# Optimization experiments

Hardware: AMD Instinct MI355X
Metric: run time of the kernel (lower is better)

## Reference

```python
import jax, jax.numpy as jnp
import numpy as np

B, N, E, H, L = 1, 1024, 32, 1024, 8  # batch, num concepts, dim_edge, dim_hidden, stack_len


def setup_inputs() -> dict:
    key = jax.random.key(0)
    k = jax.random.split(key, 12)
    vision_feat = jax.random.normal(k[0], (B, 36, H), jnp.float32)   # unused by forward
    feat = jax.random.normal(k[1], (B, N - 1, N, E), jnp.float32)
    feat_edge = jax.random.normal(k[2], (B, 1, N, E), jnp.float32)
    c_i = jax.random.normal(k[3], (B, H), jnp.float32)
    relation_mask = jnp.ones((B, N), jnp.float32)                    # only its size is read
    att_stack = jax.random.uniform(k[4], (B, N, N, L), dtype=jnp.float32)
    sp = jax.random.uniform(k[5], (B, L), dtype=jnp.float32)
    stack_ptr = sp / jnp.sum(sp, axis=-1, keepdims=True)             # soft stack pointer
    mem_in = jax.random.normal(k[6], (B, H), jnp.float32)
    mono_mask = (jax.random.uniform(k[7], (B, N, N, 1)) > 0.5).astype(jnp.float32)
    cross_mask = jax.random.uniform(k[8], (E,), dtype=jnp.float32)
    w_c = jax.random.normal(k[9], (E, H), jnp.float32) / np.sqrt(H).astype(np.float32)
    b_c = jax.random.normal(k[10], (E,), jnp.float32) * 0.01
    return {"vision_feat": vision_feat, "feat": feat, "feat_edge": feat_edge,
            "c_i": c_i, "relation_mask": relation_mask, "att_stack": att_stack,
            "stack_ptr": stack_ptr, "mem_in": mem_in, "mono_mask": mono_mask,
            "cross_mask": cross_mask, "w_c": w_c, "b_c": b_c}


def reference(vision_feat, feat, feat_edge, c_i, relation_mask, att_stack,
              stack_ptr, mem_in, mono_mask, cross_mask, w_c, b_c):
    b = feat_edge.shape[0]
    # query = map_c(c_i).view(B,1,1,-1).expand_as(feat_edge)
    query = (c_i @ w_c.T + b_c).reshape(b, 1, 1, -1)
    query = jnp.broadcast_to(query, feat_edge.shape)                 # (B,1,N,E)
    I = jnp.concatenate([query, feat], axis=1)                       # (B,N,N,E)
    # Fusion: -(x-y)^2 + relu(x+y), feat_edge broadcasts over dim1
    elt_prod = -(I - feat_edge) ** 2 + jax.nn.relu(I + feat_edge)    # (B,N,N,E)
    weit_matrix = mono_mask * elt_prod                               # (B,N,N,E)
    # soft stack read + permute(0,2,1): att_in[b,y,x] = sum_l att_stack[b,x,y,l]*ptr[b,l]
    att_in = jnp.einsum('bxyl,bl->byx', att_stack, stack_ptr)        # (B,N,N)
    # (att_in @ weit_matrix) @ cross_mask, then permute(0,2,1).
    # Contract the edge dim first (mathematically identical by linearity).
    wv = jnp.einsum('bmye,e->bmy', weit_matrix, cross_mask)          # (B,N,N)
    att_out = jnp.einsum('bxy,bmy->bxm', att_in, wv)                 # (B,N,N)
    # max-normalize with detached norm clamped to >= 1
    norm = jax.lax.stop_gradient(jnp.max(att_out, axis=1, keepdims=True))
    norm = jnp.where(norm <= 1, jnp.ones_like(norm), norm)
    att_out = att_out / norm
    # soft stack write
    ptr = stack_ptr[:, None, None, :]                                # (B,1,1,L)
    att_stack_new = att_out[..., None] * ptr + att_stack * (1 - ptr) # (B,N,N,L)
    return att_stack_new, stack_ptr, jnp.zeros_like(mem_in)
```

## Files before the change

kernel.cpp:

```cpp
#include <hip/hip_runtime.h>
#include <math.h>

#define N 1024
#define E 32
#define L 8
#define NN ((size_t)N * N)

using short8 = __attribute__((ext_vector_type(8))) short;
using f32x4v = __attribute__((ext_vector_type(4))) float;

__device__ inline ushort2 split_bf16(float v) {
  unsigned ui = __float_as_uint(v);
  ushort h = (ushort)(ui >> 16);
  float hv = __uint_as_float((unsigned)h << 16);
  float r = v - hv;
  ushort l = (ushort)(__float_as_uint(r) >> 16);
  return make_ushort2(h, l);
}

__device__ inline void gload16(const void* g, void* l) {
  __builtin_amdgcn_global_load_lds(
      (const __attribute__((address_space(1))) unsigned int*)g,
      (__attribute__((address_space(3))) unsigned int*)l, 16, 0, 0);
}

__global__ __launch_bounds__(256) void k_prep(
    const float* __restrict__ feat, const float* __restrict__ fe,
    const float* __restrict__ mono, const float* __restrict__ cm,
    const float* __restrict__ c_i, const float* __restrict__ w_c,
    const float* __restrict__ b_c,
    const float* __restrict__ att_stack, const float* __restrict__ ptr,
    ushort* __restrict__ wv_h, ushort* __restrict__ wv_l,
    ushort* __restrict__ Pt_h, ushort* __restrict__ Pt_l,
    float* __restrict__ out_tail) {
  __shared__ __align__(16) float qsm[32];
  __shared__ ushort Ts[2][64][66];
  int tid = threadIdx.x;
  int b = blockIdx.x;
  if (b < 8192) {
    int seg = tid & 7;
    int rl = tid >> 3;
    bool qblock = (b < 8);
    if (qblock) {
      int e = tid >> 3, r = tid & 7;
      float s = 0.f;
      for (int h = r; h < N; h += 8) s += c_i[h] * w_c[e * N + h];
      s += __shfl_down(s, 4, 8);
      s += __shfl_down(s, 2, 8);
      s += __shfl_down(s, 1, 8);
      if (r == 0) qsm[e] = s + b_c[e];
      __syncthreads();
    }
    float4 c = *(const float4*)(cm + seg * 4);
    float4 qa;
    if (qblock) qa = *((const float4*)qsm + seg);
    #pragma unroll
    for (int it = 0; it < 4; ++it) {
      int gid = b * 128 + it * 32 + rl;
      int m = gid >> 10;
      int y = gid & (N - 1);
      float4 a;
      if (qblock) {
        a = qa;
      } else {
        a = *(const float4*)(feat + ((size_t)(m - 1) * N + y) * E + seg * 4);
      }
      float4 f = *(const float4*)(fe + (size_t)y * E + seg * 4);
      float dx = a.x - f.x, dy = a.y - f.y, dz = a.z - f.z, dw = a.w - f.w;
      float s = c.x * (fmaxf(a.x + f.x, 0.f) - dx * dx)
              + c.y * (fmaxf(a.y + f.y, 0.f) - dy * dy)
              + c.z * (fmaxf(a.z + f.z, 0.f) - dz * dz)
              + c.w * (fmaxf(a.w + f.w, 0.f) - dw * dw);
      s += __shfl_down(s, 4, 8);
      s += __shfl_down(s, 2, 8);
      s += __shfl_down(s, 1, 8);
      if (seg == 0) {
        float v = mono[gid] * s;
        ushort2 hl = split_bf16(v);
        wv_h[gid] = hl.x;
        wv_l[gid] = hl.y;
      }
    }
  } else if (b < 8448) {
    int b2 = b - 8192;
    int j0 = (b2 >> 4) * 64;
    int i0 = (b2 & 15) * 64;
    float p0 = ptr[0], p1 = ptr[1], p2 = ptr[2], p3 = ptr[3];
    float p4 = ptr[4], p5 = ptr[5], p6 = ptr[6], p7 = ptr[7];
    int w = tid >> 6, lane = tid & 63;
    #pragma unroll 4
    for (int r = 0; r < 16; ++r) {
      int jl = r * 4 + w;
      int il = lane;
      const float4* a =
          (const float4*)(att_stack + ((size_t)(j0 + jl) * N + i0 + il) * L);
      float4 a0 = a[0], a1 = a[1];
      float s = a0.x * p0 + a0.y * p1 + a0.z * p2 + a0.w * p3
              + a1.x * p4 + a1.y * p5 + a1.z * p6 + a1.w * p7;
      ushort2 hl = split_bf16(s);
      Ts[0][il][jl] = hl.x;
      Ts[1][il][jl] = hl.y;
    }
    __syncthreads();
    int il = tid >> 2, cc = tid & 3;
    size_t o = (size_t)(i0 + il) * N + j0 + cc * 16;
    {
      const uint* sp = (const uint*)&Ts[0][il][cc * 16];
      uint4 d0 = {sp[0], sp[1], sp[2], sp[3]};
      uint4 d1 = {sp[4], sp[5], sp[6], sp[7]};
      *(uint4*)&Pt_h[o] = d0;
      *(uint4*)&Pt_h[o + 8] = d1;
    }
    {
      const uint* sp = (const uint*)&Ts[1][il][cc * 16];
      uint4 d0 = {sp[0], sp[1], sp[2], sp[3]};
      uint4 d1 = {sp[4], sp[5], sp[6], sp[7]};
      *(uint4*)&Pt_l[o] = d0;
      *(uint4*)&Pt_l[o + 8] = d1;
    }
  } else {
    if (tid < 8) out_tail[tid] = ptr[tid];
    for (int i = tid; i < N; i += 256) out_tail[8 + i] = 0.f;
  }
}

__global__ __launch_bounds__(256) void k_mm(
    const ushort* __restrict__ Pt_h, const ushort* __restrict__ Pt_l,
    const ushort* __restrict__ wv_h, const ushort* __restrict__ wv_l,
    float* __restrict__ C, float* __restrict__ normp) {
  __shared__ ushort As[2][2][64][32];
  __shared__ ushort Bs[2][2][64][32];
  __shared__ float nm[64][17];
  int tid = threadIdx.x;
  int lane = tid & 63, w = tid >> 6;
  int x0 = blockIdx.x * 64, m0 = blockIdx.y * 64;
  int srow = w * 16 + (lane >> 2);
  int gsrc = (((lane & 3) ^ ((lane >> 3) & 3))) * 8;
  const ushort* gAh = Pt_h + (size_t)(x0 + srow) * N + gsrc;
  const ushort* gAl = Pt_l + (size_t)(x0 + srow) * N + gsrc;
  const ushort* gBh = wv_h + (size_t)(m0 + srow) * N + gsrc;
  const ushort* gBl = wv_l + (size_t)(m0 + srow) * N + gsrc;
  int fr = w * 16 + (lane & 15);
  int fn = lane & 15;
  int grn = ((lane >> 4) ^ ((lane >> 1) & 3)) << 4;
  f32x4v acc[4];
  #pragma unroll
  for (int t = 0; t < 4; ++t) acc[t] = (f32x4v){0.f, 0.f, 0.f, 0.f};
  gload16(gAh, &As[0][0][w * 16][0]);
  gload16(gAl, &As[0][1][w * 16][0]);
  gload16(gBh, &Bs[0][0][w * 16][0]);
  gload16(gBl, &Bs[0][1][w * 16][0]);
  #pragma unroll 2
  for (int kt = 0; kt < 32; ++kt) {
    int cur = kt & 1;
    __syncthreads();
    if (kt < 31) {
      int nxt = cur ^ 1;
      gload16(gAh + (kt + 1) * 32, &As[nxt][0][w * 16][0]);
      gload16(gAl + (kt + 1) * 32, &As[nxt][1][w * 16][0]);
      gload16(gBh + (kt + 1) * 32, &Bs[nxt][0][w * 16][0]);
      gload16(gBl + (kt + 1) * 32, &Bs[nxt][1][w * 16][0]);
    }
    const char* aB0 = (const char*)&As[cur][0][0][0];
    const char* aB1 = (const char*)&As[cur][1][0][0];
    short8 Ah = *(const short8*)(aB0 + fr * 64 + grn);
    short8 Al = *(const short8*)(aB1 + fr * 64 + grn);
    const char* bB0 = (const char*)&Bs[cur][0][0][0];
    const char* bB1 = (const char*)&Bs[cur][1][0][0];
    #pragma unroll
    for (int t = 0; t < 4; ++t) {
      short8 Bh = *(const short8*)(bB0 + (t * 16 + fn) * 64 + grn);
      short8 Bl = *(const short8*)(bB1 + (t * 16 + fn) * 64 + grn);
      acc[t] = __builtin_amdgcn_mfma_f32_16x16x32_bf16(Ah, Bh, acc[t], 0, 0, 0);
      acc[t] = __builtin_amdgcn_mfma_f32_16x16x32_bf16(Ah, Bl, acc[t], 0, 0, 0);
      acc[t] = __builtin_amdgcn_mfma_f32_16x16x32_bf16(Al, Bh, acc[t], 0, 0, 0);
    }
  }
  int orow = x0 + w * 16 + (lane >> 4) * 4;
  int ocol = m0 + fn;
  int cidx = w * 4 + (lane >> 4);
  #pragma unroll
  for (int t = 0; t < 4; ++t) {
    float mx = -INFINITY;
    #pragma unroll
    for (int r = 0; r < 4; ++r) {
      float v = acc[t][r];
      C[(size_t)(orow + r) * N + ocol + t * 16] = v;
      mx = fmaxf(mx, v);
    }
    nm[t * 16 + fn][cidx] = mx;
  }
  __syncthreads();
  if (tid < 64) {
    float mx = nm[tid][0];
    #pragma unroll
    for (int j = 1; j < 16; ++j) mx = fmaxf(mx, nm[tid][j]);
    normp[(size_t)blockIdx.x * N + m0 + tid] = mx;
  }
}

__global__ __launch_bounds__(256) void k_fin(
    const float* __restrict__ C, const float* __restrict__ normp,
    const float* __restrict__ att_stack, const float* __restrict__ ptr,
    float* __restrict__ out) {
  int gid = blockIdx.x * 256 + threadIdx.x;
  int m = gid & (N - 1);
  float mx = normp[m];
  #pragma unroll
  for (int xg = 1; xg < 16; ++xg)
    mx = fmaxf(mx, normp[(size_t)xg * N + m]);
  float nrm = (mx <= 1.f) ? 1.f : mx;
  float a = C[gid] / nrm;
  const float4* s = (const float4*)(att_stack + (size_t)gid * L);
  float4 s0 = s[0], s1 = s[1];
  float p0 = ptr[0], p1 = ptr[1], p2 = ptr[2], p3 = ptr[3];
  float p4 = ptr[4], p5 = ptr[5], p6 = ptr[6], p7 = ptr[7];
  float4 o0, o1;
  o0.x = a * p0 + s0.x * (1.f - p0);
  o0.y = a * p1 + s0.y * (1.f - p1);
  o0.z = a * p2 + s0.z * (1.f - p2);
  o0.w = a * p3 + s0.w * (1.f - p3);
  o1.x = a * p4 + s1.x * (1.f - p4);
  o1.y = a * p5 + s1.y * (1.f - p5);
  o1.z = a * p6 + s1.z * (1.f - p6);
  o1.w = a * p7 + s1.w * (1.f - p7);
  float4* o = (float4*)(out + (size_t)gid * L);
  o[0] = o0;
  o[1] = o1;
}

extern "C" void kernel_launch(void* const* d_in, const int* in_sizes, int n_in,
                              void* d_out, int out_size, void* d_ws, size_t ws_size,
                              hipStream_t stream) {
  const float* feat      = (const float*)d_in[1];
  const float* feat_edge = (const float*)d_in[2];
  const float* c_i       = (const float*)d_in[3];
  const float* att_stack = (const float*)d_in[5];
  const float* stack_ptr = (const float*)d_in[6];
  const float* mono_mask = (const float*)d_in[8];
  const float* cross_mask= (const float*)d_in[9];
  const float* w_c       = (const float*)d_in[10];
  const float* b_c       = (const float*)d_in[11];

  float* out = (float*)d_out;

  ushort* wv_h = (ushort*)d_ws;
  ushort* wv_l = wv_h + NN;
  ushort* Pt_h = wv_l + NN;
  ushort* Pt_l = Pt_h + NN;
  float*  C    = (float*)(Pt_l + NN);
  float*  normp= C + NN;

  float* out_tail = out + NN * L;

  k_prep<<<8449, 256, 0, stream>>>(feat, feat_edge, mono_mask, cross_mask,
                                   c_i, w_c, b_c, att_stack, stack_ptr,
                                   wv_h, wv_l, Pt_h, Pt_l, out_tail);
  dim3 mmgrid(16, 16);
  k_mm<<<mmgrid, 256, 0, stream>>>(Pt_h, Pt_l, wv_h, wv_l, C, normp);
  k_fin<<<4096, 256, 0, stream>>>(C, normp, att_stack, stack_ptr, out);
}
```

Measured before the change: 280.3 us.

## Load GEMM fragments directly into registers with 4-stage prefetch; split finalize per half-row

The split-bf16 GEMM no longer stages A/B tiles through LDS with global_load_lds and a barrier on every k-step. Each wave now loads its MFMA fragments straight from global memory into registers, keeping four k-steps in flight as a software pipeline, which removes the LDS traffic and __syncthreads. In exchange, register pressure rises sharply (4 stages of 10 short8 vectors), and the B fragments are reloaded redundantly by each of the four waves instead of being shared through LDS. The finalize kernel now uses two threads per element, each doing one float4, doubling the thread count to get more coalesced and parallel memory access.

```diff
diff --git a/kernel.cpp b/kernel.cpp
--- a/kernel.cpp
+++ b/kernel.cpp
@@ -16,12 +16,6 @@
   float r = v - hv;
   ushort l = (ushort)(__float_as_uint(r) >> 16);
   return make_ushort2(h, l);
-}
-
-__device__ inline void gload16(const void* g, void* l) {
-  __builtin_amdgcn_global_load_lds(
-      (const __attribute__((address_space(1))) unsigned int*)g,
-      (__attribute__((address_space(3))) unsigned int*)l, 16, 0, 0);
 }
 
 __global__ __launch_bounds__(256) void k_prep(
@@ -128,56 +122,60 @@
     const ushort* __restrict__ Pt_h, const ushort* __restrict__ Pt_l,
     const ushort* __restrict__ wv_h, const ushort* __restrict__ wv_l,
     float* __restrict__ C, float* __restrict__ normp) {
-  __shared__ ushort As[2][2][64][32];
-  __shared__ ushort Bs[2][2][64][32];
   __shared__ float nm[64][17];
   int tid = threadIdx.x;
   int lane = tid & 63, w = tid >> 6;
   int x0 = blockIdx.x * 64, m0 = blockIdx.y * 64;
-  int srow = w * 16 + (lane >> 2);
-  int gsrc = (((lane & 3) ^ ((lane >> 3) & 3))) * 8;
-  const ushort* gAh = Pt_h + (size_t)(x0 + srow) * N + gsrc;
-  const ushort* gAl = Pt_l + (size_t)(x0 + srow) * N + gsrc;
-  const ushort* gBh = wv_h + (size_t)(m0 + srow) * N + gsrc;
-  const ushort* gBl = wv_l + (size_t)(m0 + srow) * N + gsrc;
-  int fr = w * 16 + (lane & 15);
-  int fn = lane & 15;
-  int grn = ((lane >> 4) ^ ((lane >> 1) & 3)) << 4;
+  int fr = lane & 15;
+  int fk = (lane >> 4) * 8;
+  const ushort* pAh = Pt_h + (size_t)(x0 + w * 16 + fr) * N + fk;
+  const ushort* pAl = Pt_l + (size_t)(x0 + w * 16 + fr) * N + fk;
+  size_t br0 = (size_t)(m0 + 0 * 16 + fr) * N + fk;
+  size_t br1 = (size_t)(m0 + 1 * 16 + fr) * N + fk;
+  size_t br2 = (size_t)(m0 + 2 * 16 + fr) * N + fk;
+  size_t br3 = (size_t)(m0 + 3 * 16 + fr) * N + fk;
+
+  short8 Ah[4], Al[4], Bh[4][4], Bl[4][4];
+
+#define LOADK(s, kt)                                                   \
+  do {                                                                 \
+    const int ko = (kt) * 32;                                          \
+    Ah[s] = *(const short8*)(pAh + ko);                                \
+    Al[s] = *(const short8*)(pAl + ko);                                \
+    Bh[s][0] = *(const short8*)(wv_h + br0 + ko);                      \
+    Bl[s][0] = *(const short8*)(wv_l + br0 + ko);                      \
+    Bh[s][1] = *(const short8*)(wv_h + br1 + ko);                      \
+    Bl[s][1] = *(const short8*)(wv_l + br1 + ko);                      \
+    Bh[s][2] = *(const short8*)(wv_h + br2 + ko);                      \
+    Bl[s][2] = *(const short8*)(wv_l + br2 + ko);                      \
+    Bh[s][3] = *(const short8*)(wv_h + br3 + ko);                      \
+    Bl[s][3] = *(const short8*)(wv_l + br3 + ko);                      \
+  } while (0)
+
   f32x4v acc[4];
   #pragma unroll
   for (int t = 0; t < 4; ++t) acc[t] = (f32x4v){0.f, 0.f, 0.f, 0.f};
-  gload16(gAh, &As[0][0][w * 16][0]);
-  gload16(gAl, &As[0][1][w * 16][0]);
-  gload16(gBh, &Bs[0][0][w * 16][0]);
-  gload16(gBl, &Bs[0][1][w * 16][0]);
-  #pragma unroll 2
+
+  LOADK(0, 0);
+  LOADK(1, 1);
+  LOADK(2, 2);
+  LOADK(3, 3);
+
+  #pragma unroll
   for (int kt = 0; kt < 32; ++kt) {
-    int cur = kt & 1;
-    __syncthreads();
-    if (kt < 31) {
-      int nxt = cur ^ 1;
-      gload16(gAh + (kt + 1) * 32, &As[nxt][0][w * 16][0]);
-      gload16(gAl + (kt + 1) * 32, &As[nxt][1][w * 16][0]);
-      gload16(gBh + (kt + 1) * 32, &Bs[nxt][0][w * 16][0]);
-      gload16(gBl + (kt + 1) * 32, &Bs[nxt][1][w * 16][0]);
-    }
-    const char* aB0 = (const char*)&As[cur][0][0][0];
-    const char* aB1 = (const char*)&As[cur][1][0][0];
-    short8 Ah = *(const short8*)(aB0 + fr * 64 + grn);
-    short8 Al = *(const short8*)(aB1 + fr * 64 + grn);
-    const char* bB0 = (const char*)&Bs[cur][0][0][0];
-    const char* bB1 = (const char*)&Bs[cur][1][0][0];
+    const int s = kt & 3;
     #pragma unroll
     for (int t = 0; t < 4; ++t) {
-      short8 Bh = *(const short8*)(bB0 + (t * 16 + fn) * 64 + grn);
-      short8 Bl = *(const short8*)(bB1 + (t * 16 + fn) * 64 + grn);
-      acc[t] = __builtin_amdgcn_mfma_f32_16x16x32_bf16(Ah, Bh, acc[t], 0, 0, 0);
-      acc[t] = __builtin_amdgcn_mfma_f32_16x16x32_bf16(Ah, Bl, acc[t], 0, 0, 0);
-      acc[t] = __builtin_amdgcn_mfma_f32_16x16x32_bf16(Al, Bh, acc[t], 0, 0, 0);
-    }
-  }
+      acc[t] = __builtin_amdgcn_mfma_f32_16x16x32_bf16(Ah[s], Bh[s][t], acc[t], 0, 0, 0);
+      acc[t] = __builtin_amdgcn_mfma_f32_16x16x32_bf16(Ah[s], Bl[s][t], acc[t], 0, 0, 0);
+      acc[t] = __builtin_amdgcn_mfma_f32_16x16x32_bf16(Al[s], Bh[s][t], acc[t], 0, 0, 0);
+    }
+    if (kt < 28) LOADK(s, kt + 4);
+  }
+#undef LOADK
+
   int orow = x0 + w * 16 + (lane >> 4) * 4;
-  int ocol = m0 + fn;
+  int ocol = m0 + fr;
   int cidx = w * 4 + (lane >> 4);
   #pragma unroll
   for (int t = 0; t < 4; ++t) {
@@ -188,7 +186,7 @@
       C[(size_t)(orow + r) * N + ocol + t * 16] = v;
       mx = fmaxf(mx, v);
     }
-    nm[t * 16 + fn][cidx] = mx;
+    nm[t * 16 + fr][cidx] = mx;
   }
   __syncthreads();
   if (tid < 64) {
@@ -203,30 +201,24 @@
     const float* __restrict__ C, const float* __restrict__ normp,
     const float* __restrict__ att_stack, const float* __restrict__ ptr,
     float* __restrict__ out) {
-  int gid = blockIdx.x * 256 + threadIdx.x;
+  int f = blockIdx.x * 256 + threadIdx.x;
+  int gid = f >> 1;
   int m = gid & (N - 1);
+  int h = f & 1;
   float mx = normp[m];
   #pragma unroll
   for (int xg = 1; xg < 16; ++xg)
     mx = fmaxf(mx, normp[(size_t)xg * N + m]);
   float nrm = (mx <= 1.f) ? 1.f : mx;
   float a = C[gid] / nrm;
-  const float4* s = (const float4*)(att_stack + (size_t)gid * L);
-  float4 s0 = s[0], s1 = s[1];
-  float p0 = ptr[0], p1 = ptr[1], p2 = ptr[2], p3 = ptr[3];
-  float p4 = ptr[4], p5 = ptr[5], p6 = ptr[6], p7 = ptr[7];
-  float4 o0, o1;
-  o0.x = a * p0 + s0.x * (1.f - p0);
-  o0.y = a * p1 + s0.y * (1.f - p1);
-  o0.z = a * p2 + s0.z * (1.f - p2);
-  o0.w = a * p3 + s0.w * (1.f - p3);
-  o1.x = a * p4 + s1.x * (1.f - p4);
-  o1.y = a * p5 + s1.y * (1.f - p5);
-  o1.z = a * p6 + s1.z * (1.f - p6);
-  o1.w = a * p7 + s1.w * (1.f - p7);
-  float4* o = (float4*)(out + (size_t)gid * L);
-  o[0] = o0;
-  o[1] = o1;
+  float4 s0 = ((const float4*)att_stack)[f];
+  float4 p = ((const float4*)ptr)[h];
+  float4 o0;
+  o0.x = a * p.x + s0.x * (1.f - p.x);
+  o0.y = a * p.y + s0.y * (1.f - p.y);
+  o0.z = a * p.z + s0.z * (1.f - p.z);
+  o0.w = a * p.w + s0.w * (1.f - p.w);
+  ((float4*)out)[f] = o0;
 }
 
 extern "C" void kernel_launch(void* const* d_in, const int* in_sizes, int n_in,
@@ -258,5 +250,5 @@
                                    wv_h, wv_l, Pt_h, Pt_l, out_tail);
   dim3 mmgrid(16, 16);
   k_mm<<<mmgrid, 256, 0, stream>>>(Pt_h, Pt_l, wv_h, wv_l, C, normp);
-  k_fin<<<4096, 256, 0, stream>>>(C, normp, att_stack, stack_ptr, out);
-}
+  k_fin<<<8192, 256, 0, stream>>>(C, normp, att_stack, stack_ptr, out);
+}
```

Measured after the change: 298.9 us. 1.07x slower.

## Fuse finalize into matmul via cooperative grid sync, drop C buffer

Applied to the files above, without the earlier changes.

Merges the normalization and stack-write kernel into the matmul kernel. A cooperative grid-wide sync lets each block read the global column max, and the block then writes the output directly from its accumulators. This removes the intermediate C matrix write and read, plus one kernel launch. The trade-off is that the bandwidth-heavy stack update now runs on only 256 blocks, with a grid barrier, which may reduce memory-level parallelism.

```diff
diff --git a/kernel.cpp b/kernel.cpp
--- a/kernel.cpp
+++ b/kernel.cpp
@@ -1,5 +1,8 @@
 #include <hip/hip_runtime.h>
+#include <hip/hip_cooperative_groups.h>
 #include <math.h>
+
+namespace cg = cooperative_groups;
 
 #define N 1024
 #define E 32
@@ -127,10 +130,12 @@
 __global__ __launch_bounds__(256) void k_mm(
     const ushort* __restrict__ Pt_h, const ushort* __restrict__ Pt_l,
     const ushort* __restrict__ wv_h, const ushort* __restrict__ wv_l,
-    float* __restrict__ C, float* __restrict__ normp) {
+    float* __restrict__ normp, const float* __restrict__ att_stack,
+    const float* __restrict__ ptr, float* __restrict__ out) {
   __shared__ ushort As[2][2][64][32];
   __shared__ ushort Bs[2][2][64][32];
   __shared__ float nm[64][17];
+  __shared__ float nrm64[64];
   int tid = threadIdx.x;
   int lane = tid & 63, w = tid >> 6;
   int x0 = blockIdx.x * 64, m0 = blockIdx.y * 64;
@@ -176,18 +181,10 @@
       acc[t] = __builtin_amdgcn_mfma_f32_16x16x32_bf16(Al, Bh, acc[t], 0, 0, 0);
     }
   }
-  int orow = x0 + w * 16 + (lane >> 4) * 4;
-  int ocol = m0 + fn;
   int cidx = w * 4 + (lane >> 4);
   #pragma unroll
   for (int t = 0; t < 4; ++t) {
-    float mx = -INFINITY;
-    #pragma unroll
-    for (int r = 0; r < 4; ++r) {
-      float v = acc[t][r];
-      C[(size_t)(orow + r) * N + ocol + t * 16] = v;
-      mx = fmaxf(mx, v);
-    }
+    float mx = fmaxf(fmaxf(acc[t][0], acc[t][1]), fmaxf(acc[t][2], acc[t][3]));
     nm[t * 16 + fn][cidx] = mx;
   }
   __syncthreads();
@@ -197,36 +194,45 @@
     for (int j = 1; j < 16; ++j) mx = fmaxf(mx, nm[tid][j]);
     normp[(size_t)blockIdx.x * N + m0 + tid] = mx;
   }
-}
-
-__global__ __launch_bounds__(256) void k_fin(
-    const float* __restrict__ C, const float* __restrict__ normp,
-    const float* __restrict__ att_stack, const float* __restrict__ ptr,
-    float* __restrict__ out) {
-  int gid = blockIdx.x * 256 + threadIdx.x;
-  int m = gid & (N - 1);
-  float mx = normp[m];
-  #pragma unroll
-  for (int xg = 1; xg < 16; ++xg)
-    mx = fmaxf(mx, normp[(size_t)xg * N + m]);
-  float nrm = (mx <= 1.f) ? 1.f : mx;
-  float a = C[gid] / nrm;
-  const float4* s = (const float4*)(att_stack + (size_t)gid * L);
-  float4 s0 = s[0], s1 = s[1];
+  cg::this_grid().sync();
+  if (tid < 64) {
+    int m = m0 + tid;
+    float mx = normp[m];
+    #pragma unroll
+    for (int xg = 1; xg < 16; ++xg)
+      mx = fmaxf(mx, normp[(size_t)xg * N + m]);
+    nrm64[tid] = (mx <= 1.f) ? 1.f : mx;
+  }
+  __syncthreads();
   float p0 = ptr[0], p1 = ptr[1], p2 = ptr[2], p3 = ptr[3];
   float p4 = ptr[4], p5 = ptr[5], p6 = ptr[6], p7 = ptr[7];
-  float4 o0, o1;
-  o0.x = a * p0 + s0.x * (1.f - p0);
-  o0.y = a * p1 + s0.y * (1.f - p1);
-  o0.z = a * p2 + s0.z * (1.f - p2);
-  o0.w = a * p3 + s0.w * (1.f - p3);
-  o1.x = a * p4 + s1.x * (1.f - p4);
-  o1.y = a * p5 + s1.y * (1.f - p5);
-  o1.z = a * p6 + s1.z * (1.f - p6);
-  o1.w = a * p7 + s1.w * (1.f - p7);
-  float4* o = (float4*)(out + (size_t)gid * L);
-  o[0] = o0;
-  o[1] = o1;
+  float q0 = 1.f - p0, q1 = 1.f - p1, q2 = 1.f - p2, q3 = 1.f - p3;
+  float q4 = 1.f - p4, q5 = 1.f - p5, q6 = 1.f - p6, q7 = 1.f - p7;
+  int orow = x0 + w * 16 + (lane >> 4) * 4;
+  #pragma unroll
+  for (int t = 0; t < 4; ++t) {
+    float rn = 1.f / nrm64[t * 16 + fn];
+    int ocol = m0 + t * 16 + fn;
+    #pragma unroll
+    for (int r = 0; r < 4; ++r) {
+      float a = acc[t][r] * rn;
+      size_t base = ((size_t)(orow + r) * N + ocol) * L;
+      const float4* s = (const float4*)(att_stack + base);
+      float4 s0 = s[0], s1 = s[1];
+      float4 o0, o1;
+      o0.x = a * p0 + s0.x * q0;
+      o0.y = a * p1 + s0.y * q1;
+      o0.z = a * p2 + s0.z * q2;
+      o0.w = a * p3 + s0.w * q3;
+      o1.x = a * p4 + s1.x * q4;
+      o1.y = a * p5 + s1.y * q5;
+      o1.z = a * p6 + s1.z * q6;
+      o1.w = a * p7 + s1.w * q7;
+      float4* o = (float4*)(out + base);
+      o[0] = o0;
+      o[1] = o1;
+    }
+  }
 }
 
 extern "C" void kernel_launch(void* const* d_in, const int* in_sizes, int n_in,
@@ -248,15 +254,17 @@
   ushort* wv_l = wv_h + NN;
   ushort* Pt_h = wv_l + NN;
   ushort* Pt_l = Pt_h + NN;
-  float*  C    = (float*)(Pt_l + NN);
-  float*  normp= C + NN;
+  float*  normp= (float*)(Pt_l + NN);
 
   float* out_tail = out + NN * L;
 
   k_prep<<<8449, 256, 0, stream>>>(feat, feat_edge, mono_mask, cross_mask,
                                    c_i, w_c, b_c, att_stack, stack_ptr,
                                    wv_h, wv_l, Pt_h, Pt_l, out_tail);
-  dim3 mmgrid(16, 16);
-  k_mm<<<mmgrid, 256, 0, stream>>>(Pt_h, Pt_l, wv_h, wv_l, C, normp);
-  k_fin<<<4096, 256, 0, stream>>>(C, normp, att_stack, stack_ptr, out);
-}
+
+  void* args[] = {(void*)&Pt_h, (void*)&Pt_l, (void*)&wv_h, (void*)&wv_l,
+                  (void*)&normp, (void*)&att_stack, (void*)&stack_ptr,
+                  (void*)&out};
+  hipLaunchCooperativeKernel((const void*)k_mm, dim3(16, 16), dim3(256),
+                             args, 0, stream);
+}
```

New measurement: 331.2 us. +18.1%, slower.

## Drop split-bf16 compensation to single rounded bf16 and retile GEMM to 32x32

Applied to the files above, without the earlier changes.

The split-bf16 (hi/lo) representation of both GEMM operands is replaced by a single round-to-nearest-even bf16 value, so the matmul needs one MFMA per k-step instead of three and the prep kernel writes half as many bytes. The GEMM tile shrinks from 64x64 to 32x32, giving a 32x32 grid with one MFMA tile per wave, and the final kernel now reduces 32 partial column maxima. The result loses the extra precision the lo terms supplied, which may push the error past the tolerance for a 1024-long fp32 reduction.

```diff
diff --git a/kernel.cpp b/kernel.cpp
--- a/kernel.cpp
+++ b/kernel.cpp
@@ -9,13 +9,9 @@
 using short8 = __attribute__((ext_vector_type(8))) short;
 using f32x4v = __attribute__((ext_vector_type(4))) float;
 
-__device__ inline ushort2 split_bf16(float v) {
-  unsigned ui = __float_as_uint(v);
-  ushort h = (ushort)(ui >> 16);
-  float hv = __uint_as_float((unsigned)h << 16);
-  float r = v - hv;
-  ushort l = (ushort)(__float_as_uint(r) >> 16);
-  return make_ushort2(h, l);
+__device__ inline ushort bf16_rtne(float v) {
+  unsigned u = __float_as_uint(v);
+  return (ushort)((u + 0x7FFF + ((u >> 16) & 1)) >> 16);
 }
 
 __device__ inline void gload16(const void* g, void* l) {
@@ -30,11 +26,10 @@
     const float* __restrict__ c_i, const float* __restrict__ w_c,
     const float* __restrict__ b_c,
     const float* __restrict__ att_stack, const float* __restrict__ ptr,
-    ushort* __restrict__ wv_h, ushort* __restrict__ wv_l,
-    ushort* __restrict__ Pt_h, ushort* __restrict__ Pt_l,
+    ushort* __restrict__ wv, ushort* __restrict__ Pt,
     float* __restrict__ out_tail) {
   __shared__ __align__(16) float qsm[32];
-  __shared__ ushort Ts[2][64][66];
+  __shared__ ushort Ts[64][66];
   int tid = threadIdx.x;
   int b = blockIdx.x;
   if (b < 8192) {
@@ -75,10 +70,7 @@
       s += __shfl_down(s, 2, 8);
       s += __shfl_down(s, 1, 8);
       if (seg == 0) {
-        float v = mono[gid] * s;
-        ushort2 hl = split_bf16(v);
-        wv_h[gid] = hl.x;
-        wv_l[gid] = hl.y;
+        wv[gid] = bf16_rtne(mono[gid] * s);
       }
     }
   } else if (b < 8448) {
@@ -97,27 +89,16 @@
       float4 a0 = a[0], a1 = a[1];
       float s = a0.x * p0 + a0.y * p1 + a0.z * p2 + a0.w * p3
               + a1.x * p4 + a1.y * p5 + a1.z * p6 + a1.w * p7;
-      ushort2 hl = split_bf16(s);
-      Ts[0][il][jl] = hl.x;
-      Ts[1][il][jl] = hl.y;
+      Ts[il][jl] = bf16_rtne(s);
     }
     __syncthreads();
     int il = tid >> 2, cc = tid & 3;
     size_t o = (size_t)(i0 + il) * N + j0 + cc * 16;
-    {
-      const uint* sp = (const uint*)&Ts[0][il][cc * 16];
-      uint4 d0 = {sp[0], sp[1], sp[2], sp[3]};
-      uint4 d1 = {sp[4], sp[5], sp[6], sp[7]};
-      *(uint4*)&Pt_h[o] = d0;
-      *(uint4*)&Pt_h[o + 8] = d1;
-    }
-    {
-      const uint* sp = (const uint*)&Ts[1][il][cc * 16];
-      uint4 d0 = {sp[0], sp[1], sp[2], sp[3]};
-      uint4 d1 = {sp[4], sp[5], sp[6], sp[7]};
-      *(uint4*)&Pt_l[o] = d0;
-      *(uint4*)&Pt_l[o + 8] = d1;
-    }
+    const uint* sp = (const uint*)&Ts[il][cc * 16];
+    uint4 d0 = {sp[0], sp[1], sp[2], sp[3]};
+    uint4 d1 = {sp[4], sp[5], sp[6], sp[7]};
+    *(uint4*)&Pt[o] = d0;
+    *(uint4*)&Pt[o + 8] = d1;
   } else {
     if (tid < 8) out_tail[tid] = ptr[tid];
     for (int i = tid; i < N; i += 256) out_tail[8 + i] = 0.f;
@@ -125,77 +106,60 @@
 }
 
 __global__ __launch_bounds__(256) void k_mm(
-    const ushort* __restrict__ Pt_h, const ushort* __restrict__ Pt_l,
-    const ushort* __restrict__ wv_h, const ushort* __restrict__ wv_l,
+    const ushort* __restrict__ Pt, const ushort* __restrict__ wv,
     float* __restrict__ C, float* __restrict__ normp) {
-  __shared__ ushort As[2][2][64][32];
-  __shared__ ushort Bs[2][2][64][32];
-  __shared__ float nm[64][17];
+  __shared__ ushort As[2][32][32];
+  __shared__ ushort Bs[2][32][32];
+  __shared__ float nm[32][9];
   int tid = threadIdx.x;
   int lane = tid & 63, w = tid >> 6;
-  int x0 = blockIdx.x * 64, m0 = blockIdx.y * 64;
-  int srow = w * 16 + (lane >> 2);
-  int gsrc = (((lane & 3) ^ ((lane >> 3) & 3))) * 8;
-  const ushort* gAh = Pt_h + (size_t)(x0 + srow) * N + gsrc;
-  const ushort* gAl = Pt_l + (size_t)(x0 + srow) * N + gsrc;
-  const ushort* gBh = wv_h + (size_t)(m0 + srow) * N + gsrc;
-  const ushort* gBl = wv_l + (size_t)(m0 + srow) * N + gsrc;
-  int fr = w * 16 + (lane & 15);
-  int fn = lane & 15;
-  int grn = ((lane >> 4) ^ ((lane >> 1) & 3)) << 4;
-  f32x4v acc[4];
-  #pragma unroll
-  for (int t = 0; t < 4; ++t) acc[t] = (f32x4v){0.f, 0.f, 0.f, 0.f};
-  gload16(gAh, &As[0][0][w * 16][0]);
-  gload16(gAl, &As[0][1][w * 16][0]);
-  gload16(gBh, &Bs[0][0][w * 16][0]);
-  gload16(gBl, &Bs[0][1][w * 16][0]);
+  int x0 = blockIdx.x * 32, m0 = blockIdx.y * 32;
+  int srow = (w & 1) * 16 + (lane >> 2);
+  int gsrc = ((lane & 3) ^ ((lane >> 3) & 3)) * 8;
+  const ushort* gp = (w < 2) ? Pt + (size_t)(x0 + srow) * N + gsrc
+                             : wv + (size_t)(m0 + srow) * N + gsrc;
+  int wr = w >> 1, wc = w & 1;
+  int fr = lane & 15;
+  int grn = ((lane >> 4) ^ ((fr >> 1) & 3)) << 4;
+  const char* aBase = (const char*)&As[0][0][0];
+  const char* bBase = (const char*)&Bs[0][0][0];
+  int aOff = (wr * 16 + fr) * 64 + grn;
+  int bOff = (wc * 16 + fr) * 64 + grn;
+  f32x4v acc = (f32x4v){0.f, 0.f, 0.f, 0.f};
+  {
+    ushort* dst = (w < 2) ? &As[0][(w & 1) * 16][0] : &Bs[0][(w & 1) * 16][0];
+    gload16(gp, dst);
+  }
   #pragma unroll 2
   for (int kt = 0; kt < 32; ++kt) {
     int cur = kt & 1;
     __syncthreads();
     if (kt < 31) {
       int nxt = cur ^ 1;
-      gload16(gAh + (kt + 1) * 32, &As[nxt][0][w * 16][0]);
-      gload16(gAl + (kt + 1) * 32, &As[nxt][1][w * 16][0]);
-      gload16(gBh + (kt + 1) * 32, &Bs[nxt][0][w * 16][0]);
-      gload16(gBl + (kt + 1) * 32, &Bs[nxt][1][w * 16][0]);
-    }
-    const char* aB0 = (const char*)&As[cur][0][0][0];
-    const char* aB1 = (const char*)&As[cur][1][0][0];
-    short8 Ah = *(const short8*)(aB0 + fr * 64 + grn);
-    short8 Al = *(const short8*)(aB1 + fr * 64 + grn);
-    const char* bB0 = (const char*)&Bs[cur][0][0][0];
-    const char* bB1 = (const char*)&Bs[cur][1][0][0];
+      ushort* dst = (w < 2) ? &As[nxt][(w & 1) * 16][0]
+                            : &Bs[nxt][(w & 1) * 16][0];
+      gload16(gp + (kt + 1) * 32, dst);
+    }
+    short8 Av = *(const short8*)(aBase + cur * 2048 + aOff);
+    short8 Bv = *(const short8*)(bBase + cur * 2048 + bOff);
+    acc = __builtin_amdgcn_mfma_f32_16x16x32_bf16(Av, Bv, acc, 0, 0, 0);
+  }
+  int orow = x0 + wr * 16 + (lane >> 4) * 4;
+  int ocol = m0 + wc * 16 + fr;
+  float mx = -INFINITY;
+  #pragma unroll
+  for (int r = 0; r < 4; ++r) {
+    float v = acc[r];
+    C[(size_t)(orow + r) * N + ocol] = v;
+    mx = fmaxf(mx, v);
+  }
+  nm[wc * 16 + fr][wr * 4 + (lane >> 4)] = mx;
+  __syncthreads();
+  if (tid < 32) {
+    float m2 = nm[tid][0];
     #pragma unroll
-    for (int t = 0; t < 4; ++t) {
-      short8 Bh = *(const short8*)(bB0 + (t * 16 + fn) * 64 + grn);
-      short8 Bl = *(const short8*)(bB1 + (t * 16 + fn) * 64 + grn);
-      acc[t] = __builtin_amdgcn_mfma_f32_16x16x32_bf16(Ah, Bh, acc[t], 0, 0, 0);
-      acc[t] = __builtin_amdgcn_mfma_f32_16x16x32_bf16(Ah, Bl, acc[t], 0, 0, 0);
-      acc[t] = __builtin_amdgcn_mfma_f32_16x16x32_bf16(Al, Bh, acc[t], 0, 0, 0);
-    }
-  }
-  int orow = x0 + w * 16 + (lane >> 4) * 4;
-  int ocol = m0 + fn;
-  int cidx = w * 4 + (lane >> 4);
-  #pragma unroll
-  for (int t = 0; t < 4; ++t) {
-    float mx = -INFINITY;
-    #pragma unroll
-    for (int r = 0; r < 4; ++r) {
-      float v = acc[t][r];
-      C[(size_t)(orow + r) * N + ocol + t * 16] = v;
-      mx = fmaxf(mx, v);
-    }
-    nm[t * 16 + fn][cidx] = mx;
-  }
-  __syncthreads();
-  if (tid < 64) {
-    float mx = nm[tid][0];
-    #pragma unroll
-    for (int j = 1; j < 16; ++j) mx = fmaxf(mx, nm[tid][j]);
-    normp[(size_t)blockIdx.x * N + m0 + tid] = mx;
+    for (int j = 1; j < 8; ++j) m2 = fmaxf(m2, nm[tid][j]);
+    normp[(size_t)blockIdx.x * N + m0 + tid] = m2;
   }
 }
 
@@ -207,7 +171,7 @@
   int m = gid & (N - 1);
   float mx = normp[m];
   #pragma unroll
-  for (int xg = 1; xg < 16; ++xg)
+  for (int xg = 1; xg < 32; ++xg)
     mx = fmaxf(mx, normp[(size_t)xg * N + m]);
   float nrm = (mx <= 1.f) ? 1.f : mx;
   float a = C[gid] / nrm;
@@ -244,19 +208,17 @@
 
   float* out = (float*)d_out;
 
-  ushort* wv_h = (ushort*)d_ws;
-  ushort* wv_l = wv_h + NN;
-  ushort* Pt_h = wv_l + NN;
-  ushort* Pt_l = Pt_h + NN;
-  float*  C    = (float*)(Pt_l + NN);
+  ushort* wv   = (ushort*)d_ws;
+  ushort* Pt   = wv + NN;
+  float*  C    = (float*)(Pt + NN);
   float*  normp= C + NN;
 
   float* out_tail = out + NN * L;
 
   k_prep<<<8449, 256, 0, stream>>>(feat, feat_edge, mono_mask, cross_mask,
                                    c_i, w_c, b_c, att_stack, stack_ptr,
-                                   wv_h, wv_l, Pt_h, Pt_l, out_tail);
-  dim3 mmgrid(16, 16);
-  k_mm<<<mmgrid, 256, 0, stream>>>(Pt_h, Pt_l, wv_h, wv_l, C, normp);
+                                   wv, Pt, out_tail);
+  dim3 mmgrid(32, 32);
+  k_mm<<<mmgrid, 256, 0, stream>>>(Pt, wv, C, normp);
   k_fin<<<4096, 256, 0, stream>>>(C, normp, att_stack, stack_ptr, out);
 }
```

Result: no change. 275.2 us (-1.8%).
